# Optimization experiments

Hardware: AMD Instinct MI355X
Metric: run time of the kernel (lower is better)

Reference implementation:

```python
import jax, jax.numpy as jnp
import numpy as np

DIM = 512
HEADS = 8
HD = DIM // HEADS
WS = 4          # window_size
SHIFT = 2       # window_size // 2
HID = 4 * DIM   # mlp hidden
EPS = 1e-5


def _ln(x, g, b):
    m = jnp.mean(x, axis=-1, keepdims=True)
    v = jnp.mean((x - m) ** 2, axis=-1, keepdims=True)
    return (x - m) * jax.lax.rsqrt(v + EPS) * g + b


def setup_inputs() -> dict:
    key = jax.random.key(0)
    ks = jax.random.split(key, 12)
    s = 0.02
    return {
        "x": jax.random.normal(ks[0], (2, 32, 32, 32, DIM), dtype=jnp.float32),
        "ln1_g": jnp.ones((DIM,), jnp.float32),
        "ln1_b": jnp.zeros((DIM,), jnp.float32),
        "qkv_w": jax.random.normal(ks[1], (DIM, 3 * DIM), jnp.float32) * s,
        "qkv_b": jnp.zeros((3 * DIM,), jnp.float32),
        "proj_w": jax.random.normal(ks[2], (DIM, DIM), jnp.float32) * s,
        "proj_b": jnp.zeros((DIM,), jnp.float32),
        "ln2_g": jnp.ones((DIM,), jnp.float32),
        "ln2_b": jnp.zeros((DIM,), jnp.float32),
        "ffn_w1": jax.random.normal(ks[3], (DIM, HID), jnp.float32) * s,
        "ffn_b1": jnp.zeros((HID,), jnp.float32),
        "ffn_w2": jax.random.normal(ks[4], (HID, DIM), jnp.float32) * s,
        "ffn_b2": jnp.zeros((DIM,), jnp.float32),
    }


def reference(x, ln1_g, ln1_b, qkv_w, qkv_b, proj_w, proj_b,
              ln2_g, ln2_b, ffn_w1, ffn_b1, ffn_w2, ffn_b2):
    B, D, H, W, C = x.shape
    nD, nH, nW = D // WS, H // WS, W // WS
    N = WS ** 3

    # cyclic shift
    xs = jnp.roll(x, (-SHIFT, -SHIFT, -SHIFT), axis=(1, 2, 3))

    # window partition: (B*numWin, N, C)
    xw = xs.reshape(B, nD, WS, nH, WS, nW, WS, C)
    xw = xw.transpose(0, 1, 3, 5, 2, 4, 6, 7).reshape(-1, N, C)

    # pre-norm attention
    h = _ln(xw, ln1_g, ln1_b)
    qkv = (h @ qkv_w + qkv_b).reshape(-1, N, 3, HEADS, HD)
    q, k, v = jnp.moveaxis(qkv, 2, 0)          # each (Bn, N, HEADS, HD)
    scale = HD ** -0.5
    logits = jnp.einsum('bnhd,bmhd->bhnm', q, k) * scale
    attn = jax.nn.softmax(logits, axis=-1)
    out = jnp.einsum('bhnm,bmhd->bnhd', attn, v).reshape(-1, N, C)
    out = out @ proj_w + proj_b
    xw = xw + out

    # window reverse + unshift
    xo = xw.reshape(B, nD, nH, nW, WS, WS, WS, C)
    xo = xo.transpose(0, 1, 4, 2, 5, 3, 6, 7).reshape(B, D, H, W, C)
    xo = jnp.roll(xo, (SHIFT, SHIFT, SHIFT), axis=(1, 2, 3))

    # pre-norm FFN (exact GELU, dropout inactive in eval)
    h2 = _ln(xo, ln2_g, ln2_b)
    ffn = jax.nn.gelu(h2 @ ffn_w1 + ffn_b1, approximate=False) @ ffn_w2 + ffn_b2
    return xo + ffn
```

## Files before the change

### kernel.cpp

```cpp
#include <hip/hip_runtime.h>
#include <hip/hip_bf16.h>


typedef __attribute__((ext_vector_type(4))) short short4v;
typedef __attribute__((ext_vector_type(8))) short short8v;
typedef __attribute__((ext_vector_type(4))) float f32x4;

__device__ __forceinline__ unsigned short f2bf(float f) {
  unsigned u = __float_as_uint(f);
  u += 0x7fffu + ((u >> 16) & 1u);
  return (unsigned short)(u >> 16);
}

__device__ __forceinline__ float erf_fast(float x) {
  float ax = fabsf(x);
  float y = 1.0f + 0.3275911f * ax;
  float t;
  asm("v_rcp_f32 %0, %1" : "=v"(t) : "v"(y));
  float p = t * (0.254829592f +
            t * (-0.284496736f +
            t * (1.421413741f +
            t * (-1.453152027f +
            t * 1.061405429f))));
  float e = __expf(-ax * ax);
  float r = 1.0f - p * e;
  return copysignf(r, x);
}

__device__ __forceinline__ void gload_lds16(const unsigned short* g, unsigned short* l) {
  __builtin_amdgcn_global_load_lds(
      (const __attribute__((address_space(1))) unsigned int*)g,
      (__attribute__((address_space(3))) unsigned int*)l, 16, 0, 0);
}

__global__ __launch_bounds__(256)
void wprep_all(const float* __restrict__ qkv_w, const float* __restrict__ proj_w,
               const float* __restrict__ w1, const float* __restrict__ w2,
               unsigned short* __restrict__ wt) {
  int idx = blockIdx.x * 256 + threadIdx.x;
  const float* w; int kbits, N, base;
  if (idx < 786432)       { w = qkv_w;  kbits = 9;  N = 1536; base = 0; }
  else if (idx < 1048576) { w = proj_w; kbits = 9;  N = 512;  base = 786432; }
  else if (idx < 2097152) { w = w1;     kbits = 9;  N = 2048; base = 1048576; }
  else                    { w = w2;     kbits = 11; N = 512;  base = 2097152; }
  int li = idx - base;
  int K = 1 << kbits;
  int n = li >> kbits, kk = li & (K - 1);
  wt[idx] = f2bf(w[(long)kk * N + n]);
}

__global__ __launch_bounds__(256)
void ln_kernel(const float* __restrict__ src, const float* __restrict__ g,
               const float* __restrict__ bb, unsigned short* __restrict__ dst,
               const int gather) {
  const int lane = threadIdx.x & 63;
  const int row = blockIdx.x * 4 + (threadIdx.x >> 6);
  long srow;
  if (gather) {
    int n = row & 63, win = row >> 6;
    int w0 = win & 7, h0 = (win >> 3) & 7, d0 = (win >> 6) & 7, b2 = win >> 9;
    int dx = n & 3, dy = (n >> 2) & 3, dz = n >> 4;
    int od = (d0 * 4 + dz + 2) & 31, oh = (h0 * 4 + dy + 2) & 31, ow = (w0 * 4 + dx + 2) & 31;
    srow = (((long)b2 * 32 + od) * 32 + oh) * 32 + ow;
  } else {
    srow = row;
  }
  const float4* sp = (const float4*)(src + srow * 512);
  float4 x0 = sp[lane], x1 = sp[lane + 64];
  float sum = x0.x + x0.y + x0.z + x0.w + x1.x + x1.y + x1.z + x1.w;
  float sq  = x0.x*x0.x + x0.y*x0.y + x0.z*x0.z + x0.w*x0.w
            + x1.x*x1.x + x1.y*x1.y + x1.z*x1.z + x1.w*x1.w;
#pragma unroll
  for (int off = 1; off < 64; off <<= 1) {
    sum += __shfl_xor(sum, off, 64);
    sq  += __shfl_xor(sq, off, 64);
  }
  float mean = sum * (1.0f / 512.0f);
  float var  = sq * (1.0f / 512.0f) - mean * mean;
  float rstd = rsqrtf(var + 1e-5f);
  float4 g0 = ((const float4*)g)[lane], g1 = ((const float4*)g)[lane + 64];
  float4 b0 = ((const float4*)bb)[lane], b1v = ((const float4*)bb)[lane + 64];
  ushort4 o0, o1;
  o0.x = f2bf((x0.x - mean) * rstd * g0.x + b0.x);
  o0.y = f2bf((x0.y - mean) * rstd * g0.y + b0.y);
  o0.z = f2bf((x0.z - mean) * rstd * g0.z + b0.z);
  o0.w = f2bf((x0.w - mean) * rstd * g0.w + b0.w);
  o1.x = f2bf((x1.x - mean) * rstd * g1.x + b1v.x);
  o1.y = f2bf((x1.y - mean) * rstd * g1.y + b1v.y);
  o1.z = f2bf((x1.z - mean) * rstd * g1.z + b1v.z);
  o1.w = f2bf((x1.w - mean) * rstd * g1.w + b1v.w);
  *(ushort4*)(dst + (long)row * 512 + lane * 4) = o0;
  *(ushort4*)(dst + (long)row * 512 + 256 + lane * 4) = o1;
}

template <int EPI>
__global__ __launch_bounds__(512, 2)
void gemm_bt(const unsigned short* __restrict__ A,
             const unsigned short* __restrict__ Bt,
             const float* __restrict__ bias, int K,
             void* __restrict__ out0,
             unsigned short* __restrict__ out1,
             unsigned short* __restrict__ out2,
             const float* __restrict__ res) {
  __shared__ unsigned short As[2][256 * 64];
  __shared__ unsigned short Bs[2][256 * 64];
  const int tid = threadIdx.x;
  const int lane = tid & 63;
  const int wv = tid >> 6;
  const int wm = wv >> 2;
  const int wn = wv & 3;
  const int quad = lane >> 4;
  const int l15 = lane & 15;

  const int gx = gridDim.x;
  const int nwg = gx * gridDim.y;
  const int bid = blockIdx.y * gx + blockIdx.x;
  const int cpx = nwg >> 3;
  const int wg2 = (bid & 7) * cpx + (bid >> 3);
  const int bx = wg2 % gx;
  const int by = wg2 / gx;
  const long row0 = (long)by * 256;
  const long col0 = (long)bx * 256;

  f32x4 acc[8][4] = {};

  const int srow = wv * 8 + (lane >> 3);
  const int scg  = (lane & 7) ^ (lane >> 3);
  const unsigned short* gA = A  + (row0 + srow) * K + scg * 8;
  const unsigned short* gB = Bt + (col0 + srow) * K + scg * 8;
  const long jmp = 64L * K;
  const int ldst = wv * 512;

#define STAGE_A(buf, koff) do {                                         \
    _Pragma("unroll")                                                   \
    for (int j = 0; j < 4; ++j)                                         \
      gload_lds16(gA + (koff) + j * jmp, &As[buf][ldst + j * 4096]);    \
  } while (0)
#define STAGE_B(buf, koff) do {                                         \
    _Pragma("unroll")                                                   \
    for (int j = 0; j < 4; ++j)                                         \
      gload_lds16(gB + (koff) + j * jmp, &Bs[buf][ldst + j * 4096]);    \
  } while (0)

  const int co0 = ((quad)     ^ (l15 & 7)) * 8;
  const int co1 = ((quad + 4) ^ (l15 & 7)) * 8;
  const int aB0 = (wm * 128 + l15) * 64 + co0;
  const int aB1 = (wm * 128 + l15) * 64 + co1;
  const int bB0 = (wn * 64 + l15) * 64 + co0;
  const int bB1 = (wn * 64 + l15) * 64 + co1;

  const int nk = K >> 6;
  STAGE_A(0, 0);
  STAGE_B(0, 0);
  __syncthreads();

  for (int t = 0; t < nk; ++t) {
    const int cur = t & 1, nxt = cur ^ 1;
    const unsigned short* Ac = As[cur];
    const unsigned short* Bc = Bs[cur];
    if (t + 1 < nk) {
      const int kn = (t + 1) << 6;
      STAGE_A(nxt, kn);
      STAGE_B(nxt, kn);
    }
    short8v bf0[4], bf1[4];
#pragma unroll
    for (int nt = 0; nt < 4; ++nt) {
      bf0[nt] = *(const short8v*)&Bc[bB0 + nt * 1024];
      bf1[nt] = *(const short8v*)&Bc[bB1 + nt * 1024];
    }
#pragma unroll
    for (int mh = 0; mh < 2; ++mh) {
      short8v af0[4], af1[4];
#pragma unroll
      for (int i = 0; i < 4; ++i) {
        af0[i] = *(const short8v*)&Ac[aB0 + (mh * 4 + i) * 1024];
        af1[i] = *(const short8v*)&Ac[aB1 + (mh * 4 + i) * 1024];
      }
      __builtin_amdgcn_s_setprio(1);
#pragma unroll
      for (int i = 0; i < 4; ++i)
#pragma unroll
        for (int nt = 0; nt < 4; ++nt)
          acc[mh * 4 + i][nt] = __builtin_amdgcn_mfma_f32_16x16x32_bf16(
              af0[i], bf0[nt], acc[mh * 4 + i][nt], 0, 0, 0);
#pragma unroll
      for (int i = 0; i < 4; ++i)
#pragma unroll
        for (int nt = 0; nt < 4; ++nt)
          acc[mh * 4 + i][nt] = __builtin_amdgcn_mfma_f32_16x16x32_bf16(
              af1[i], bf1[nt], acc[mh * 4 + i][nt], 0, 0, 0);
      __builtin_amdgcn_s_setprio(0);
    }
    __syncthreads();
  }
#undef STAGE_A
#undef STAGE_B

#pragma unroll
  for (int mt = 0; mt < 8; ++mt) {
#pragma unroll
    for (int nt = 0; nt < 4; ++nt) {
#pragma unroll
      for (int r = 0; r < 4; ++r) {
        const long gr = row0 + wm * 128 + mt * 16 + quad * 4 + r;
        const long gc = col0 + wn * 64 + nt * 16 + l15;
        float val = acc[mt][nt][r] + bias[gc];
        if (EPI == 0) {
          int which = (int)(gc >> 9), rem = (int)gc & 511;
          int head = rem >> 6, hd = rem & 63;
          long win = gr >> 6, n = gr & 63;
          long base = (win * 8 + head) * 4096;
          unsigned short bv = f2bf(val);
          if (which == 0)      ((unsigned short*)out0)[base + n * 64 + hd] = bv;
          else if (which == 1) out1[base + n * 64 + hd] = bv;
          else                 out2[base + hd * 64 + n] = bv;
        } else if (EPI == 1) {
          int win = (int)(gr >> 6), n = (int)gr & 63;
          int w0 = win & 7, h0 = (win >> 3) & 7, d0 = (win >> 6) & 7, b2 = win >> 9;
          int dx = n & 3, dy = (n >> 2) & 3, dz = n >> 4;
          int od = (d0 * 4 + dz + 2) & 31, oh = (h0 * 4 + dy + 2) & 31, ow = (w0 * 4 + dx + 2) & 31;
          long addr = ((((long)b2 * 32 + od) * 32 + oh) * 32 + ow) * 512 + gc;
          ((float*)out0)[addr] = res[addr] + val;
        } else if (EPI == 2) {
          float ge = 0.5f * val * (1.0f + erf_fast(val * 0.70710678118654752f));
          ((unsigned short*)out0)[gr * 2048 + gc] = f2bf(ge);
        } else {
          long addr = gr * 512 + gc;
          ((float*)out0)[addr] = res[addr] + val;
        }
      }
    }
  }
}

__global__ __launch_bounds__(256)
void attn_kernel(const unsigned short* __restrict__ q,
                 const unsigned short* __restrict__ k,
                 const unsigned short* __restrict__ vt,
                 unsigned short* __restrict__ out) {
  __shared__ unsigned short Ps[4][64 * 72];
  const int lane = threadIdx.x & 63;
  const int wave = threadIdx.x >> 6;
  const int quad = lane >> 4;
  const int l15 = lane & 15;
  const int unit = blockIdx.x * 4 + wave;
  const int win = unit >> 3;
  const int head = unit & 7;
  const long base = (long)unit * 4096;

  f32x4 s[4][4] = {};
#pragma unroll
  for (int kk = 0; kk < 64; kk += 32) {
    short8v a[4], b[4];
#pragma unroll
    for (int t = 0; t < 4; ++t) {
      a[t] = *(const short8v*)(q + base + (t * 16 + l15) * 64 + kk + quad * 8);
      b[t] = *(const short8v*)(k + base + (t * 16 + l15) * 64 + kk + quad * 8);
    }
#pragma unroll
    for (int mt = 0; mt < 4; ++mt)
#pragma unroll
      for (int nt = 0; nt < 4; ++nt)
        s[mt][nt] = __builtin_amdgcn_mfma_f32_16x16x32_bf16(a[mt], b[nt], s[mt][nt], 0, 0, 0);
  }

  float lrow[4][4];
#pragma unroll
  for (int mt = 0; mt < 4; ++mt) {
#pragma unroll
    for (int r = 0; r < 4; ++r) {
      float v0 = s[mt][0][r] * 0.125f, v1 = s[mt][1][r] * 0.125f;
      float v2 = s[mt][2][r] * 0.125f, v3 = s[mt][3][r] * 0.125f;
      float mx = fmaxf(fmaxf(v0, v1), fmaxf(v2, v3));
#pragma unroll
      for (int off = 1; off < 16; off <<= 1) mx = fmaxf(mx, __shfl_xor(mx, off, 64));
      v0 = __expf(v0 - mx); v1 = __expf(v1 - mx);
      v2 = __expf(v2 - mx); v3 = __expf(v3 - mx);
      float sm = v0 + v1 + v2 + v3;
#pragma unroll
      for (int off = 1; off < 16; off <<= 1) sm += __shfl_xor(sm, off, 64);
      lrow[mt][r] = sm;
      int row = mt * 16 + quad * 4 + r;
      Ps[wave][row * 72 + 0 + l15]  = f2bf(v0);
      Ps[wave][row * 72 + 16 + l15] = f2bf(v1);
      Ps[wave][row * 72 + 32 + l15] = f2bf(v2);
      Ps[wave][row * 72 + 48 + l15] = f2bf(v3);
    }
  }
  __syncthreads();

  f32x4 o[4][4] = {};
#pragma unroll
  for (int kk = 0; kk < 64; kk += 32) {
    short8v a[4], b[4];
#pragma unroll
    for (int t = 0; t < 4; ++t) {
      a[t] = *(const short8v*)(&Ps[wave][(t * 16 + l15) * 72 + kk + quad * 8]);
      b[t] = *(const short8v*)(vt + base + (t * 16 + l15) * 64 + kk + quad * 8);
    }
#pragma unroll
    for (int mt = 0; mt < 4; ++mt)
#pragma unroll
      for (int nt = 0; nt < 4; ++nt)
        o[mt][nt] = __builtin_amdgcn_mfma_f32_16x16x32_bf16(a[mt], b[nt], o[mt][nt], 0, 0, 0);
  }

#pragma unroll
  for (int mt = 0; mt < 4; ++mt)
#pragma unroll
    for (int nt = 0; nt < 4; ++nt)
#pragma unroll
      for (int r = 0; r < 4; ++r) {
        int row = mt * 16 + quad * 4 + r;
        int col = nt * 16 + l15;
        float val = o[mt][nt][r] / lrow[mt][r];
        out[((long)win * 64 + row) * 512 + head * 64 + col] = f2bf(val);
      }
}

extern "C" void kernel_launch(void* const* d_in, const int* in_sizes, int n_in,
                              void* d_out, int out_size, void* d_ws, size_t ws_size,
                              hipStream_t stream) {
  const float* x      = (const float*)d_in[0];
  const float* ln1_g  = (const float*)d_in[1];
  const float* ln1_b  = (const float*)d_in[2];
  const float* qkv_w  = (const float*)d_in[3];
  const float* qkv_b  = (const float*)d_in[4];
  const float* proj_w = (const float*)d_in[5];
  const float* proj_b = (const float*)d_in[6];
  const float* ln2_g  = (const float*)d_in[7];
  const float* ln2_b  = (const float*)d_in[8];
  const float* w1     = (const float*)d_in[9];
  const float* b1     = (const float*)d_in[10];
  const float* w2     = (const float*)d_in[11];
  const float* b2     = (const float*)d_in[12];

  char* ws = (char*)d_ws;
  unsigned short* wt_all  = (unsigned short*)ws;
  unsigned short* wt_qkv  = (unsigned short*)(ws + 0);
  unsigned short* wt_proj = (unsigned short*)(ws + 1572864);
  unsigned short* wt_1    = (unsigned short*)(ws + 2097152);
  unsigned short* wt_2    = (unsigned short*)(ws + 4194304);
  float*          xo      = (float*)(ws + 8388608);
  unsigned short* h       = (unsigned short*)(ws + 142606336);
  unsigned short* attno   = (unsigned short*)(ws + 209715200);
  unsigned short* qb      = (unsigned short*)(ws + 276824064);
  unsigned short* kb      = (unsigned short*)(ws + 343932928);
  unsigned short* vb      = (unsigned short*)(ws + 411041792);
  unsigned short* hid     = (unsigned short*)(ws + 209715200);
  float* out = (float*)d_out;

  wprep_all<<<12288, 256, 0, stream>>>(qkv_w, proj_w, w1, w2, wt_all);

  ln_kernel<<<16384, 256, 0, stream>>>(x, ln1_g, ln1_b, h, 1);
  gemm_bt<0><<<dim3(6, 256), 512, 0, stream>>>(h, wt_qkv, qkv_b, 512, qb, kb, vb, nullptr);
  attn_kernel<<<2048, 256, 0, stream>>>(qb, kb, vb, attno);
  gemm_bt<1><<<dim3(2, 256), 512, 0, stream>>>(attno, wt_proj, proj_b, 512, xo, nullptr, nullptr, x);
  ln_kernel<<<16384, 256, 0, stream>>>(xo, ln2_g, ln2_b, h, 0);
  gemm_bt<2><<<dim3(8, 256), 512, 0, stream>>>(h, wt_1, b1, 512, hid, nullptr, nullptr, nullptr);
  gemm_bt<3><<<dim3(2, 256), 512, 0, stream>>>(hid, wt_2, b2, 2048, out, nullptr, nullptr, xo);
}
```

Baseline: 1.093 ms.

## Use 4-stage K=32 LDS ring with vmcnt-based waits in GEMM

Replaces the double-buffered K=64 LDS tiles with a four-slot ring of K=32 sub-tiles. Loads are issued three stages ahead, and a counted s_waitcnt vmcnt plus a raw s_barrier replace the full __syncthreads, which keeps more global loads in flight. The LDS swizzle and addressing are redone for the 32-wide rows. LDS use per block stays the same, but each sub-step issues half the MFMAs per barrier, so there are more barriers relative to compute.

New measurement: 1.071 ms. No clear change (-2.0%).

```diff
diff --git a/kernel.cpp b/kernel.cpp
--- a/kernel.cpp
+++ b/kernel.cpp
@@ -102,8 +102,7 @@
              unsigned short* __restrict__ out1,
              unsigned short* __restrict__ out2,
              const float* __restrict__ res) {
-  __shared__ unsigned short As[2][256 * 64];
-  __shared__ unsigned short Bs[2][256 * 64];
+  __shared__ unsigned short SB[4][2][8192];
   const int tid = threadIdx.x;
   const int lane = tid & 63;
   const int wv = tid >> 6;
@@ -124,78 +123,58 @@
 
   f32x4 acc[8][4] = {};
 
-  const int srow = wv * 8 + (lane >> 3);
-  const int scg  = (lane & 7) ^ (lane >> 3);
-  const unsigned short* gA = A  + (row0 + srow) * K + scg * 8;
-  const unsigned short* gB = Bt + (col0 + srow) * K + scg * 8;
-  const long jmp = 64L * K;
-  const int ldst = wv * 512;
-
-#define STAGE_A(buf, koff) do {                                         \
-    _Pragma("unroll")                                                   \
-    for (int j = 0; j < 4; ++j)                                         \
-      gload_lds16(gA + (koff) + j * jmp, &As[buf][ldst + j * 4096]);    \
+  const int srow = wv * 16 + (lane >> 2);
+  const int scg  = (lane & 3) ^ ((lane >> 3) & 3);
+  const unsigned short* gA0 = A  + (row0 + srow) * K + scg * 8;
+  const unsigned short* gB0 = Bt + (col0 + srow) * K + scg * 8;
+  const long j1 = 128L * K;
+  const int lds0 = srow * 32 + (lane & 3) * 8;
+
+#define STAGE(v) do {                                              \
+    const int q_ = (v) & 3; const long ko_ = (long)(v) * 32;       \
+    gload_lds16(gA0 + ko_,      &SB[q_][0][lds0]);                 \
+    gload_lds16(gA0 + ko_ + j1, &SB[q_][0][lds0 + 4096]);          \
+    gload_lds16(gB0 + ko_,      &SB[q_][1][lds0]);                 \
+    gload_lds16(gB0 + ko_ + j1, &SB[q_][1][lds0 + 4096]);          \
   } while (0)
-#define STAGE_B(buf, koff) do {                                         \
-    _Pragma("unroll")                                                   \
-    for (int j = 0; j < 4; ++j)                                         \
-      gload_lds16(gB + (koff) + j * jmp, &Bs[buf][ldst + j * 4096]);    \
-  } while (0)
-
-  const int co0 = ((quad)     ^ (l15 & 7)) * 8;
-  const int co1 = ((quad + 4) ^ (l15 & 7)) * 8;
-  const int aB0 = (wm * 128 + l15) * 64 + co0;
-  const int aB1 = (wm * 128 + l15) * 64 + co1;
-  const int bB0 = (wn * 64 + l15) * 64 + co0;
-  const int bB1 = (wn * 64 + l15) * 64 + co1;
-
-  const int nk = K >> 6;
-  STAGE_A(0, 0);
-  STAGE_B(0, 0);
-  __syncthreads();
-
-  for (int t = 0; t < nk; ++t) {
-    const int cur = t & 1, nxt = cur ^ 1;
-    const unsigned short* Ac = As[cur];
-    const unsigned short* Bc = Bs[cur];
-    if (t + 1 < nk) {
-      const int kn = (t + 1) << 6;
-      STAGE_A(nxt, kn);
-      STAGE_B(nxt, kn);
-    }
-    short8v bf0[4], bf1[4];
-#pragma unroll
-    for (int nt = 0; nt < 4; ++nt) {
-      bf0[nt] = *(const short8v*)&Bc[bB0 + nt * 1024];
-      bf1[nt] = *(const short8v*)&Bc[bB1 + nt * 1024];
-    }
+
+  const int slot = (quad ^ ((l15 >> 1) & 3)) * 8;
+  const int aoff = (wm * 128 + l15) * 32 + slot;
+  const int boff = (wn * 64  + l15) * 32 + slot;
+
+  const int nsub = K >> 5;
+  STAGE(0); STAGE(1); STAGE(2);
+
+  for (int u = 0; u < nsub; ++u) {
+    if (u < nsub - 2)       asm volatile("s_waitcnt vmcnt(8)" ::: "memory");
+    else if (u == nsub - 2) asm volatile("s_waitcnt vmcnt(4)" ::: "memory");
+    else                    asm volatile("s_waitcnt vmcnt(0)" ::: "memory");
+    __builtin_amdgcn_s_barrier();
+    __builtin_amdgcn_sched_barrier(0);
+    if (u + 3 < nsub) STAGE(u + 3);
+
+    const unsigned short* Au = &SB[u & 3][0][0];
+    const unsigned short* Bu = &SB[u & 3][1][0];
+    short8v bf[4];
+#pragma unroll
+    for (int nt = 0; nt < 4; ++nt) bf[nt] = *(const short8v*)&Bu[boff + nt * 512];
 #pragma unroll
     for (int mh = 0; mh < 2; ++mh) {
-      short8v af0[4], af1[4];
-#pragma unroll
-      for (int i = 0; i < 4; ++i) {
-        af0[i] = *(const short8v*)&Ac[aB0 + (mh * 4 + i) * 1024];
-        af1[i] = *(const short8v*)&Ac[aB1 + (mh * 4 + i) * 1024];
-      }
+      short8v af[4];
+#pragma unroll
+      for (int i = 0; i < 4; ++i) af[i] = *(const short8v*)&Au[aoff + (mh * 4 + i) * 512];
       __builtin_amdgcn_s_setprio(1);
 #pragma unroll
       for (int i = 0; i < 4; ++i)
 #pragma unroll
         for (int nt = 0; nt < 4; ++nt)
           acc[mh * 4 + i][nt] = __builtin_amdgcn_mfma_f32_16x16x32_bf16(
-              af0[i], bf0[nt], acc[mh * 4 + i][nt], 0, 0, 0);
-#pragma unroll
-      for (int i = 0; i < 4; ++i)
-#pragma unroll
-        for (int nt = 0; nt < 4; ++nt)
-          acc[mh * 4 + i][nt] = __builtin_amdgcn_mfma_f32_16x16x32_bf16(
-              af1[i], bf1[nt], acc[mh * 4 + i][nt], 0, 0, 0);
+              af[i], bf[nt], acc[mh * 4 + i][nt], 0, 0, 0);
       __builtin_amdgcn_s_setprio(0);
     }
-    __syncthreads();
-  }
-#undef STAGE_A
-#undef STAGE_B
+    __builtin_amdgcn_sched_barrier(0);
+  }
+#undef STAGE
 
 #pragma unroll
   for (int mt = 0; mt < 8; ++mt) {
```
